# Kernel tuning notes

Hardware: AMD Instinct MI355X
Metric: run time of the kernel (lower is better)

## Reference

```python
import math
import jax
import jax.numpy as jnp
import numpy as np

SEGMENT_SIZE = 2048   # w (init: segment_size)
DILATION_RATE = 4     # r (init: dilation_rate)
D_MODEL = 1024        # init: d_model


def _sparse_indices(n: int, w: int, r: int, head_idx: int) -> np.ndarray:
    """Static SparsifyIndices: per segment of size w, take tokens offset::r.
    Since r divides w, every segment yields exactly m=w//r indices (no -1 pad).
    Returns flat global token indices, shape (S*m,)."""
    S = n // w
    m = w // r
    off = head_idx % r
    seg_start = np.arange(S, dtype=np.int64)[:, None] * w      # (S,1)
    within = off + r * np.arange(m, dtype=np.int64)[None, :]   # (1,m)
    return (seg_start + within).reshape(-1)


def setup_inputs() -> dict:
    key = jax.random.key(0)
    x = jax.random.normal(key, (4, 8192, D_MODEL), dtype=jnp.float32)
    return {"x": x, "head_idx": 1}


def reference(x, head_idx):
    b, n0, d = x.shape
    w, r = SEGMENT_SIZE, DILATION_RATE
    pad = (-n0) % w
    if pad:
        x = jnp.pad(x, ((0, 0), (0, pad), (0, 0)))
    n = n0 + pad
    idx = _sparse_indices(n, w, r, int(head_idx))  # static, (S*m,)
    S, m = n // w, w // r

    # Gather dilated tokens per segment: (b, S, m, d)
    xg = x[:, idx, :].reshape(b, S, m, d)

    # Softmax attention within each sub-segment (q=k=v=xg)
    scores = jnp.einsum('bsid,bsjd->bsij', xg, xg) / math.sqrt(d)  # (b,S,m,m)
    probs = jax.nn.softmax(scores, axis=-1)
    att = jnp.einsum('bsij,bsjd->bsid', probs, xg).reshape(b, S * m, d)

    # MixOutputs: alpha-weighted scatter-add back to full sequence
    denoms = att.sum(-1)                                       # (b, S*m)
    denom_sums = jnp.zeros((b, n), x.dtype).at[:, idx].add(denoms)
    alphas = denoms / denom_sums[:, idx]                       # (b, S*m)
    out = jnp.zeros((b, n, d), x.dtype).at[:, idx, :].add(att * alphas[..., None])
    return out
```

## Files before the change

### kernel.cpp

```cpp
#include <hip/hip_runtime.h>
#include <hip/hip_bf16.h>


typedef __bf16 bf16_t;
typedef __bf16 bf16x8 __attribute__((ext_vector_type(8)));
typedef float floatx4 __attribute__((ext_vector_type(4)));

#define D_MODEL 1024
#define SEG_W   2048
#define RATE    4
#define M_SUB   512
#define NTOK    8192
#define NSEGT   16
#define XG_ELEMS ((long)NSEGT * M_SUB * D_MODEL)

__device__ __forceinline__ void gload16(const bf16_t* g, bf16_t* l) {
    __builtin_amdgcn_global_load_lds(
        (const __attribute__((address_space(1))) void*)g,
        (__attribute__((address_space(3))) void*)l, 16, 0, 0);
}

__global__ __launch_bounds__(256) void gather_kernel(
    const float* __restrict__ x, const int* __restrict__ hidp,
    bf16_t* __restrict__ xg, bf16_t* __restrict__ xgT)
{
    const int off = ((hidp[0] % RATE) + RATE) % RATE;
    const int bid = blockIdx.x;
    const int seg = bid >> 7;
    const int rem = bid & 127;
    const int it  = rem >> 4;
    const int dt  = rem & 15;
    const int b   = seg >> 2, s = seg & 3;

    __shared__ ushort tile[64][65];

    const int t  = threadIdx.x;
    const int r  = t >> 2;
    const int cq = (t & 3) << 4;

    union U8 { bf16x8 v; ushort u[8]; };

    {
        const int  i   = it * 64 + r;
        const long tok = (long)s * SEG_W + off + 4L * i;
        const float* src = x + ((long)b * NTOK + tok) * D_MODEL + dt * 64 + cq;
        float4 f0 = ((const float4*)src)[0];
        float4 f1 = ((const float4*)src)[1];
        float4 f2 = ((const float4*)src)[2];
        float4 f3 = ((const float4*)src)[3];
        U8 lo, hi;
        lo.v[0]=(bf16_t)f0.x; lo.v[1]=(bf16_t)f0.y; lo.v[2]=(bf16_t)f0.z; lo.v[3]=(bf16_t)f0.w;
        lo.v[4]=(bf16_t)f1.x; lo.v[5]=(bf16_t)f1.y; lo.v[6]=(bf16_t)f1.z; lo.v[7]=(bf16_t)f1.w;
        hi.v[0]=(bf16_t)f2.x; hi.v[1]=(bf16_t)f2.y; hi.v[2]=(bf16_t)f2.z; hi.v[3]=(bf16_t)f2.w;
        hi.v[4]=(bf16_t)f3.x; hi.v[5]=(bf16_t)f3.y; hi.v[6]=(bf16_t)f3.z; hi.v[7]=(bf16_t)f3.w;
        bf16_t* dstg = xg + ((long)seg * M_SUB + i) * D_MODEL + dt * 64 + cq;
        *(bf16x8*)(dstg)     = lo.v;
        *(bf16x8*)(dstg + 8) = hi.v;
        #pragma unroll
        for (int j = 0; j < 8; ++j) { tile[r][cq + j] = lo.u[j]; tile[r][cq + 8 + j] = hi.u[j]; }
    }
    __syncthreads();
    {
        const int dc = r;
        const int iq = cq;
        U8 o0, o1;
        #pragma unroll
        for (int j = 0; j < 8; ++j) { o0.u[j] = tile[iq + j][dc]; o1.u[j] = tile[iq + 8 + j][dc]; }
        bf16_t* dstT = xgT + ((long)seg * D_MODEL + dt * 64 + dc) * M_SUB + it * 64 + iq;
        *(bf16x8*)(dstT)     = o0.v;
        *(bf16x8*)(dstT + 8) = o1.v;
    }
}

__global__ __launch_bounds__(256) void qk_kernel(
    const bf16_t* __restrict__ xg, bf16_t* __restrict__ S)
{
    const int bid = blockIdx.x;
    const int seg = bid >> 5;
    const int mt  = (bid >> 2) & 7;
    const int nt  = bid & 3;

    const int tid  = threadIdx.x;
    const int w    = tid >> 6;
    const int lane = tid & 63;
    const int l16  = lane & 15;
    const int quad = lane >> 4;
    const int wr   = w >> 1, wc = w & 1;
    const int rowin = lane >> 3;
    const int cswz  = ((lane & 7) ^ rowin) * 8;
    const int rsw   = l16 & 7;

    __shared__ alignas(16) bf16_t As[64 * 64];
    __shared__ alignas(16) bf16_t Bs[128 * 64];

    const bf16_t* xseg = xg + (long)seg * M_SUB * D_MODEL;

    const bf16_t* ga0 = xseg + (long)(mt * 64 + w * 16 + rowin) * D_MODEL + cswz;
    const bf16_t* ga1 = ga0 + 8 * D_MODEL;
    const bf16_t* gb0 = xseg + (long)(nt * 128 + w * 32 + rowin) * D_MODEL + cswz;
    const bf16_t* gb1 = gb0 +  8 * D_MODEL;
    const bf16_t* gb2 = gb0 + 16 * D_MODEL;
    const bf16_t* gb3 = gb0 + 24 * D_MODEL;
    bf16_t* la0 = &As[(w * 16 + 0) * 64];
    bf16_t* la1 = &As[(w * 16 + 8) * 64];
    bf16_t* lb0 = &Bs[(w * 32 + 0) * 64];
    bf16_t* lb1 = &Bs[(w * 32 + 8) * 64];
    bf16_t* lb2 = &Bs[(w * 32 + 16) * 64];
    bf16_t* lb3 = &Bs[(w * 32 + 24) * 64];

    floatx4 acc[2][4];
    #pragma unroll
    for (int i = 0; i < 2; ++i)
        #pragma unroll
        for (int j = 0; j < 4; ++j) acc[i][j] = (floatx4){0.f, 0.f, 0.f, 0.f};

    for (int kk = 0; kk < D_MODEL; kk += 64) {
        __syncthreads();
        gload16(ga0 + kk, la0); gload16(ga1 + kk, la1);
        gload16(gb0 + kk, lb0); gload16(gb1 + kk, lb1);
        gload16(gb2 + kk, lb2); gload16(gb3 + kk, lb3);
        __syncthreads();

        #pragma unroll
        for (int ks = 0; ks < 2; ++ks) {
            bf16x8 Af[2], Bf[4];
            #pragma unroll
            for (int m2 = 0; m2 < 2; ++m2) {
                const int row = wr * 32 + m2 * 16 + l16;
                Af[m2] = *(const bf16x8*)&As[row * 64 + (((ks * 4 + quad) ^ rsw) * 8)];
            }
            #pragma unroll
            for (int n2 = 0; n2 < 4; ++n2) {
                const int row = wc * 64 + n2 * 16 + l16;
                Bf[n2] = *(const bf16x8*)&Bs[row * 64 + (((ks * 4 + quad) ^ rsw) * 8)];
            }
            #pragma unroll
            for (int m2 = 0; m2 < 2; ++m2)
                #pragma unroll
                for (int n2 = 0; n2 < 4; ++n2)
                    acc[m2][n2] = __builtin_amdgcn_mfma_f32_16x16x32_bf16(Af[m2], Bf[n2], acc[m2][n2], 0, 0, 0);
        }
    }

    const float scale = 0.03125f;
    bf16_t* Sseg = S + (long)seg * M_SUB * M_SUB;
    #pragma unroll
    for (int m2 = 0; m2 < 2; ++m2) {
        const int qrow = mt * 64 + wr * 32 + m2 * 16 + quad * 4;
        #pragma unroll
        for (int n2 = 0; n2 < 4; ++n2) {
            const int col = nt * 128 + wc * 64 + n2 * 16 + l16;
            #pragma unroll
            for (int rg = 0; rg < 4; ++rg)
                Sseg[(long)(qrow + rg) * M_SUB + col] = (bf16_t)(acc[m2][n2][rg] * scale);
        }
    }
}

__global__ __launch_bounds__(256) void softmax_kernel(bf16_t* __restrict__ S)
{
    const int row  = blockIdx.x * 4 + (threadIdx.x >> 6);
    const int lane = threadIdx.x & 63;
    bf16_t* p = S + (long)row * M_SUB + lane * 8;
    bf16x8 v = *(const bf16x8*)p;
    float f[8];
    #pragma unroll
    for (int j = 0; j < 8; ++j) f[j] = (float)v[j];
    float m = f[0];
    #pragma unroll
    for (int j = 1; j < 8; ++j) m = fmaxf(m, f[j]);
    #pragma unroll
    for (int d = 1; d < 64; d <<= 1) m = fmaxf(m, __shfl_xor(m, d, 64));
    float sum = 0.f;
    #pragma unroll
    for (int j = 0; j < 8; ++j) { f[j] = __expf(f[j] - m); sum += f[j]; }
    #pragma unroll
    for (int d = 1; d < 64; d <<= 1) sum += __shfl_xor(sum, d, 64);
    const float inv = 1.0f / sum;
    #pragma unroll
    for (int j = 0; j < 8; ++j) v[j] = (bf16_t)(f[j] * inv);
    *(bf16x8*)p = v;
}

__global__ __launch_bounds__(256) void pv_kernel(
    const bf16_t* __restrict__ S, const bf16_t* __restrict__ xgT,
    const int* __restrict__ hidp, float* __restrict__ out)
{
    const int off = ((hidp[0] % RATE) + RATE) % RATE;
    const int bid = blockIdx.x;
    const int seg = bid >> 5;
    const int mt  = (bid >> 3) & 3;
    const int nt  = bid & 7;
    const int b   = seg >> 2, s = seg & 3;

    const int tid  = threadIdx.x;
    const int w    = tid >> 6;
    const int lane = tid & 63;
    const int l16  = lane & 15;
    const int quad = lane >> 4;
    const int wr   = w >> 1, wc = w & 1;
    const int rowin = lane >> 3;
    const int cswz  = ((lane & 7) ^ rowin) * 8;
    const int rsw   = l16 & 7;

    __shared__ alignas(16) bf16_t As[128 * 64];
    __shared__ alignas(16) bf16_t Bs[128 * 64];

    const bf16_t* Aseg = S   + (long)seg * M_SUB * M_SUB  + (long)mt * 128 * M_SUB;
    const bf16_t* Bseg = xgT + (long)seg * D_MODEL * M_SUB + (long)nt * 128 * M_SUB;

    const bf16_t* ga0 = Aseg + (long)(w * 32 + rowin) * M_SUB + cswz;
    const bf16_t* ga1 = ga0 +  8 * M_SUB;
    const bf16_t* ga2 = ga0 + 16 * M_SUB;
    const bf16_t* ga3 = ga0 + 24 * M_SUB;
    const bf16_t* gb0 = Bseg + (long)(w * 32 + rowin) * M_SUB + cswz;
    const bf16_t* gb1 = gb0 +  8 * M_SUB;
    const bf16_t* gb2 = gb0 + 16 * M_SUB;
    const bf16_t* gb3 = gb0 + 24 * M_SUB;
    bf16_t* la0 = &As[(w * 32 + 0) * 64];
    bf16_t* la1 = &As[(w * 32 + 8) * 64];
    bf16_t* la2 = &As[(w * 32 + 16) * 64];
    bf16_t* la3 = &As[(w * 32 + 24) * 64];
    bf16_t* lb0 = &Bs[(w * 32 + 0) * 64];
    bf16_t* lb1 = &Bs[(w * 32 + 8) * 64];
    bf16_t* lb2 = &Bs[(w * 32 + 16) * 64];
    bf16_t* lb3 = &Bs[(w * 32 + 24) * 64];

    floatx4 acc[4][4];
    #pragma unroll
    for (int i = 0; i < 4; ++i)
        #pragma unroll
        for (int j = 0; j < 4; ++j) acc[i][j] = (floatx4){0.f, 0.f, 0.f, 0.f};

    for (int kk = 0; kk < M_SUB; kk += 64) {
        __syncthreads();
        gload16(ga0 + kk, la0); gload16(ga1 + kk, la1);
        gload16(ga2 + kk, la2); gload16(ga3 + kk, la3);
        gload16(gb0 + kk, lb0); gload16(gb1 + kk, lb1);
        gload16(gb2 + kk, lb2); gload16(gb3 + kk, lb3);
        __syncthreads();

        #pragma unroll
        for (int ks = 0; ks < 2; ++ks) {
            bf16x8 Af[4], Bf[4];
            #pragma unroll
            for (int m2 = 0; m2 < 4; ++m2) {
                const int row = wr * 64 + m2 * 16 + l16;
                Af[m2] = *(const bf16x8*)&As[row * 64 + (((ks * 4 + quad) ^ rsw) * 8)];
            }
            #pragma unroll
            for (int n2 = 0; n2 < 4; ++n2) {
                const int row = wc * 64 + n2 * 16 + l16;
                Bf[n2] = *(const bf16x8*)&Bs[row * 64 + (((ks * 4 + quad) ^ rsw) * 8)];
            }
            #pragma unroll
            for (int m2 = 0; m2 < 4; ++m2)
                #pragma unroll
                for (int n2 = 0; n2 < 4; ++n2)
                    acc[m2][n2] = __builtin_amdgcn_mfma_f32_16x16x32_bf16(Af[m2], Bf[n2], acc[m2][n2], 0, 0, 0);
        }
    }

    float* obase = out + (long)b * NTOK * D_MODEL;
    #pragma unroll
    for (int m2 = 0; m2 < 4; ++m2) {
        const int qrow0 = mt * 128 + wr * 64 + m2 * 16 + quad * 4;
        #pragma unroll
        for (int rg = 0; rg < 4; ++rg) {
            const long tok = (long)s * SEG_W + off + 4L * (qrow0 + rg);
            float* orow = obase + tok * D_MODEL;
            #pragma unroll
            for (int n2 = 0; n2 < 4; ++n2) {
                const int d = nt * 128 + wc * 64 + n2 * 16 + l16;
                __builtin_nontemporal_store(acc[m2][n2][rg], &orow[d]);
            }
        }
    }

    {
        const floatx4 z = {0.f, 0.f, 0.f, 0.f};
        const int zr = tid >> 5;
        const int zc = tid & 31;
        #pragma unroll 4
        for (int p = 0; p < 48; ++p) {
            const int j = p * 8 + zr;
            const int q = j / 3, e = j % 3;
            const int delta = e + (e >= off ? 1 : 0);
            const long tok = (long)s * SEG_W + 4L * (mt * 128 + q) + delta;
            float* dst = obase + tok * D_MODEL + nt * 128 + zc * 4;
            __builtin_nontemporal_store(z, (floatx4*)dst);
        }
    }
}

extern "C" void kernel_launch(void* const* d_in, const int* in_sizes, int n_in,
                              void* d_out, int out_size, void* d_ws, size_t ws_size,
                              hipStream_t stream) {
    const float* x   = (const float*)d_in[0];
    const int*   hid = (const int*)d_in[1];
    float*       out = (float*)d_out;
    bf16_t* xg  = (bf16_t*)d_ws;
    bf16_t* xgT = xg + XG_ELEMS;
    bf16_t* S   = xgT + XG_ELEMS;

    gather_kernel<<<dim3(2048), dim3(256), 0, stream>>>(x, hid, xg, xgT);
    qk_kernel<<<dim3(512), dim3(256), 0, stream>>>(xg, S);
    softmax_kernel<<<dim3(2048), dim3(256), 0, stream>>>(S);
    pv_kernel<<<dim3(512), dim3(256), 0, stream>>>(S, xgT, hid, out);
}
```

Baseline: 251.1 us.

## Double-buffer LDS tiles in QK and PV GEMMs and remap block order

Both GEMM kernels switch to double-buffered shared-memory tiles: the next K-slice is loaded with global_load_lds while MFMAs consume the current buffer, with one barrier per iteration instead of two. The block index is also permuted so consecutive workgroups come from different segments, which changes how blocks spread across XCDs and their L2 caches. The aim is to hide global-load latency behind compute. In exchange, LDS use doubles, which may lower occupancy. Correctness relies on the async LDS loads having completed at the single barrier.

```diff
diff --git a/kernel.cpp b/kernel.cpp
--- a/kernel.cpp
+++ b/kernel.cpp
@@ -75,7 +75,8 @@
 __global__ __launch_bounds__(256) void qk_kernel(
     const bf16_t* __restrict__ xg, bf16_t* __restrict__ S)
 {
-    const int bid = blockIdx.x;
+    const int bid0 = blockIdx.x;
+    const int bid  = ((bid0 & 7) << 6) | (bid0 >> 3);
     const int seg = bid >> 5;
     const int mt  = (bid >> 2) & 7;
     const int nt  = bid & 3;
@@ -90,8 +91,8 @@
     const int cswz  = ((lane & 7) ^ rowin) * 8;
     const int rsw   = l16 & 7;
 
-    __shared__ alignas(16) bf16_t As[64 * 64];
-    __shared__ alignas(16) bf16_t Bs[128 * 64];
+    __shared__ alignas(16) bf16_t As[2][64 * 64];
+    __shared__ alignas(16) bf16_t Bs[2][128 * 64];
 
     const bf16_t* xseg = xg + (long)seg * M_SUB * D_MODEL;
 
@@ -101,12 +102,9 @@
     const bf16_t* gb1 = gb0 +  8 * D_MODEL;
     const bf16_t* gb2 = gb0 + 16 * D_MODEL;
     const bf16_t* gb3 = gb0 + 24 * D_MODEL;
-    bf16_t* la0 = &As[(w * 16 + 0) * 64];
-    bf16_t* la1 = &As[(w * 16 + 8) * 64];
-    bf16_t* lb0 = &Bs[(w * 32 + 0) * 64];
-    bf16_t* lb1 = &Bs[(w * 32 + 8) * 64];
-    bf16_t* lb2 = &Bs[(w * 32 + 16) * 64];
-    bf16_t* lb3 = &Bs[(w * 32 + 24) * 64];
+    const int la0 = (w * 16 + 0) * 64, la1 = (w * 16 + 8) * 64;
+    const int lb0 = (w * 32 + 0) * 64, lb1 = (w * 32 + 8) * 64;
+    const int lb2 = (w * 32 + 16) * 64, lb3 = (w * 32 + 24) * 64;
 
     floatx4 acc[2][4];
     #pragma unroll
@@ -114,25 +112,34 @@
         #pragma unroll
         for (int j = 0; j < 4; ++j) acc[i][j] = (floatx4){0.f, 0.f, 0.f, 0.f};
 
-    for (int kk = 0; kk < D_MODEL; kk += 64) {
-        __syncthreads();
-        gload16(ga0 + kk, la0); gload16(ga1 + kk, la1);
-        gload16(gb0 + kk, lb0); gload16(gb1 + kk, lb1);
-        gload16(gb2 + kk, lb2); gload16(gb3 + kk, lb3);
-        __syncthreads();
-
+    gload16(ga0, &As[0][la0]); gload16(ga1, &As[0][la1]);
+    gload16(gb0, &Bs[0][lb0]); gload16(gb1, &Bs[0][lb1]);
+    gload16(gb2, &Bs[0][lb2]); gload16(gb3, &Bs[0][lb3]);
+    __syncthreads();
+
+    for (int t = 0; t < 16; ++t) {
+        const int cur = t & 1;
+        if (t < 15) {
+            const int kk = (t + 1) * 64;
+            const int nx = cur ^ 1;
+            gload16(ga0 + kk, &As[nx][la0]); gload16(ga1 + kk, &As[nx][la1]);
+            gload16(gb0 + kk, &Bs[nx][lb0]); gload16(gb1 + kk, &Bs[nx][lb1]);
+            gload16(gb2 + kk, &Bs[nx][lb2]); gload16(gb3 + kk, &Bs[nx][lb3]);
+        }
+        const bf16_t* Ab = As[cur];
+        const bf16_t* Bb = Bs[cur];
         #pragma unroll
         for (int ks = 0; ks < 2; ++ks) {
             bf16x8 Af[2], Bf[4];
             #pragma unroll
             for (int m2 = 0; m2 < 2; ++m2) {
                 const int row = wr * 32 + m2 * 16 + l16;
-                Af[m2] = *(const bf16x8*)&As[row * 64 + (((ks * 4 + quad) ^ rsw) * 8)];
+                Af[m2] = *(const bf16x8*)&Ab[row * 64 + (((ks * 4 + quad) ^ rsw) * 8)];
             }
             #pragma unroll
             for (int n2 = 0; n2 < 4; ++n2) {
                 const int row = wc * 64 + n2 * 16 + l16;
-                Bf[n2] = *(const bf16x8*)&Bs[row * 64 + (((ks * 4 + quad) ^ rsw) * 8)];
+                Bf[n2] = *(const bf16x8*)&Bb[row * 64 + (((ks * 4 + quad) ^ rsw) * 8)];
             }
             #pragma unroll
             for (int m2 = 0; m2 < 2; ++m2)
@@ -140,6 +147,7 @@
                 for (int n2 = 0; n2 < 4; ++n2)
                     acc[m2][n2] = __builtin_amdgcn_mfma_f32_16x16x32_bf16(Af[m2], Bf[n2], acc[m2][n2], 0, 0, 0);
         }
+        __syncthreads();
     }
 
     const float scale = 0.03125f;
@@ -187,7 +195,8 @@
     const int* __restrict__ hidp, float* __restrict__ out)
 {
     const int off = ((hidp[0] % RATE) + RATE) % RATE;
-    const int bid = blockIdx.x;
+    const int bid0 = blockIdx.x;
+    const int bid  = ((bid0 & 7) << 6) | (bid0 >> 3);
     const int seg = bid >> 5;
     const int mt  = (bid >> 3) & 3;
     const int nt  = bid & 7;
@@ -203,8 +212,8 @@
     const int cswz  = ((lane & 7) ^ rowin) * 8;
     const int rsw   = l16 & 7;
 
-    __shared__ alignas(16) bf16_t As[128 * 64];
-    __shared__ alignas(16) bf16_t Bs[128 * 64];
+    __shared__ alignas(16) bf16_t As[2][128 * 64];
+    __shared__ alignas(16) bf16_t Bs[2][128 * 64];
 
     const bf16_t* Aseg = S   + (long)seg * M_SUB * M_SUB  + (long)mt * 128 * M_SUB;
     const bf16_t* Bseg = xgT + (long)seg * D_MODEL * M_SUB + (long)nt * 128 * M_SUB;
@@ -217,14 +226,8 @@
     const bf16_t* gb1 = gb0 +  8 * M_SUB;
     const bf16_t* gb2 = gb0 + 16 * M_SUB;
     const bf16_t* gb3 = gb0 + 24 * M_SUB;
-    bf16_t* la0 = &As[(w * 32 + 0) * 64];
-    bf16_t* la1 = &As[(w * 32 + 8) * 64];
-    bf16_t* la2 = &As[(w * 32 + 16) * 64];
-    bf16_t* la3 = &As[(w * 32 + 24) * 64];
-    bf16_t* lb0 = &Bs[(w * 32 + 0) * 64];
-    bf16_t* lb1 = &Bs[(w * 32 + 8) * 64];
-    bf16_t* lb2 = &Bs[(w * 32 + 16) * 64];
-    bf16_t* lb3 = &Bs[(w * 32 + 24) * 64];
+    const int la0 = (w * 32 + 0) * 64, la1 = (w * 32 + 8) * 64;
+    const int la2 = (w * 32 + 16) * 64, la3 = (w * 32 + 24) * 64;
 
     floatx4 acc[4][4];
     #pragma unroll
@@ -232,26 +235,36 @@
         #pragma unroll
         for (int j = 0; j < 4; ++j) acc[i][j] = (floatx4){0.f, 0.f, 0.f, 0.f};
 
-    for (int kk = 0; kk < M_SUB; kk += 64) {
-        __syncthreads();
-        gload16(ga0 + kk, la0); gload16(ga1 + kk, la1);
-        gload16(ga2 + kk, la2); gload16(ga3 + kk, la3);
-        gload16(gb0 + kk, lb0); gload16(gb1 + kk, lb1);
-        gload16(gb2 + kk, lb2); gload16(gb3 + kk, lb3);
-        __syncthreads();
-
+    gload16(ga0, &As[0][la0]); gload16(ga1, &As[0][la1]);
+    gload16(ga2, &As[0][la2]); gload16(ga3, &As[0][la3]);
+    gload16(gb0, &Bs[0][la0]); gload16(gb1, &Bs[0][la1]);
+    gload16(gb2, &Bs[0][la2]); gload16(gb3, &Bs[0][la3]);
+    __syncthreads();
+
+    for (int t = 0; t < 8; ++t) {
+        const int cur = t & 1;
+        if (t < 7) {
+            const int kk = (t + 1) * 64;
+            const int nx = cur ^ 1;
+            gload16(ga0 + kk, &As[nx][la0]); gload16(ga1 + kk, &As[nx][la1]);
+            gload16(ga2 + kk, &As[nx][la2]); gload16(ga3 + kk, &As[nx][la3]);
+            gload16(gb0 + kk, &Bs[nx][la0]); gload16(gb1 + kk, &Bs[nx][la1]);
+            gload16(gb2 + kk, &Bs[nx][la2]); gload16(gb3 + kk, &Bs[nx][la3]);
+        }
+        const bf16_t* Ab = As[cur];
+        const bf16_t* Bb = Bs[cur];
         #pragma unroll
         for (int ks = 0; ks < 2; ++ks) {
             bf16x8 Af[4], Bf[4];
             #pragma unroll
             for (int m2 = 0; m2 < 4; ++m2) {
                 const int row = wr * 64 + m2 * 16 + l16;
-                Af[m2] = *(const bf16x8*)&As[row * 64 + (((ks * 4 + quad) ^ rsw) * 8)];
+                Af[m2] = *(const bf16x8*)&Ab[row * 64 + (((ks * 4 + quad) ^ rsw) * 8)];
             }
             #pragma unroll
             for (int n2 = 0; n2 < 4; ++n2) {
                 const int row = wc * 64 + n2 * 16 + l16;
-                Bf[n2] = *(const bf16x8*)&Bs[row * 64 + (((ks * 4 + quad) ^ rsw) * 8)];
+                Bf[n2] = *(const bf16x8*)&Bb[row * 64 + (((ks * 4 + quad) ^ rsw) * 8)];
             }
             #pragma unroll
             for (int m2 = 0; m2 < 4; ++m2)
@@ -259,6 +272,7 @@
                 for (int n2 = 0; n2 < 4; ++n2)
                     acc[m2][n2] = __builtin_amdgcn_mfma_f32_16x16x32_bf16(Af[m2], Bf[n2], acc[m2][n2], 0, 0, 0);
         }
+        __syncthreads();
     }
 
     float* obase = out + (long)b * NTOK * D_MODEL;
```

Measured after the change: 253.6 us. Within noise of the previous version (+1.0%).

## Fuse QK, softmax and PV into a single attention kernel per query band

Applied to the files above, without the earlier changes.

Replaces the separate QK, softmax and PV kernels with one fused kernel. Each 512-thread block owns a 32-row query band, computes the full score row across 8 waves, and does the softmax with cross-wave max/sum reductions in shared memory. It keeps the probabilities in LDS for the PV matmul, so the bf16 score matrix no longer makes a round trip through global memory and two kernel launches are dropped. The fused kernel loads operands directly from global into registers with software double-buffering instead of staging them through LDS. The cost is K/V re-reads from global/L2 per band and a launch of only 256 blocks.

```diff
diff --git a/kernel.cpp b/kernel.cpp
--- a/kernel.cpp
+++ b/kernel.cpp
@@ -13,12 +13,6 @@
 #define NTOK    8192
 #define NSEGT   16
 #define XG_ELEMS ((long)NSEGT * M_SUB * D_MODEL)
-
-__device__ __forceinline__ void gload16(const bf16_t* g, bf16_t* l) {
-    __builtin_amdgcn_global_load_lds(
-        (const __attribute__((address_space(1))) void*)g,
-        (__attribute__((address_space(3))) void*)l, 16, 0, 0);
-}
 
 __global__ __launch_bounds__(256) void gather_kernel(
     const float* __restrict__ x, const int* __restrict__ hidp,
@@ -72,223 +66,223 @@
     }
 }
 
-__global__ __launch_bounds__(256) void qk_kernel(
-    const bf16_t* __restrict__ xg, bf16_t* __restrict__ S)
+__global__ __launch_bounds__(512) void attn_kernel(
+    const bf16_t* __restrict__ xg, const bf16_t* __restrict__ xgT,
+    const int* __restrict__ hidp, float* __restrict__ out)
 {
-    const int bid = blockIdx.x;
-    const int seg = bid >> 5;
-    const int mt  = (bid >> 2) & 7;
-    const int nt  = bid & 3;
+    const int off  = ((hidp[0] % RATE) + RATE) % RATE;
+    const int bid0 = blockIdx.x;
+    const int sub  = bid0 >> 3;
+    const int seg  = (bid0 & 7) * 2 + (sub >> 4);
+    const int band = sub & 15;
+    const int b = seg >> 2, s = seg & 3;
 
     const int tid  = threadIdx.x;
     const int w    = tid >> 6;
     const int lane = tid & 63;
     const int l16  = lane & 15;
     const int quad = lane >> 4;
-    const int wr   = w >> 1, wc = w & 1;
-    const int rowin = lane >> 3;
-    const int cswz  = ((lane & 7) ^ rowin) * 8;
-    const int rsw   = l16 & 7;
-
-    __shared__ alignas(16) bf16_t As[64 * 64];
-    __shared__ alignas(16) bf16_t Bs[128 * 64];
-
-    const bf16_t* xseg = xg + (long)seg * M_SUB * D_MODEL;
-
-    const bf16_t* ga0 = xseg + (long)(mt * 64 + w * 16 + rowin) * D_MODEL + cswz;
-    const bf16_t* ga1 = ga0 + 8 * D_MODEL;
-    const bf16_t* gb0 = xseg + (long)(nt * 128 + w * 32 + rowin) * D_MODEL + cswz;
-    const bf16_t* gb1 = gb0 +  8 * D_MODEL;
-    const bf16_t* gb2 = gb0 + 16 * D_MODEL;
-    const bf16_t* gb3 = gb0 + 24 * D_MODEL;
-    bf16_t* la0 = &As[(w * 16 + 0) * 64];
-    bf16_t* la1 = &As[(w * 16 + 8) * 64];
-    bf16_t* lb0 = &Bs[(w * 32 + 0) * 64];
-    bf16_t* lb1 = &Bs[(w * 32 + 8) * 64];
-    bf16_t* lb2 = &Bs[(w * 32 + 16) * 64];
-    bf16_t* lb3 = &Bs[(w * 32 + 24) * 64];
-
-    floatx4 acc[2][4];
-    #pragma unroll
-    for (int i = 0; i < 2; ++i)
-        #pragma unroll
-        for (int j = 0; j < 4; ++j) acc[i][j] = (floatx4){0.f, 0.f, 0.f, 0.f};
-
-    for (int kk = 0; kk < D_MODEL; kk += 64) {
-        __syncthreads();
-        gload16(ga0 + kk, la0); gload16(ga1 + kk, la1);
-        gload16(gb0 + kk, lb0); gload16(gb1 + kk, lb1);
-        gload16(gb2 + kk, lb2); gload16(gb3 + kk, lb3);
-        __syncthreads();
-
-        #pragma unroll
-        for (int ks = 0; ks < 2; ++ks) {
-            bf16x8 Af[2], Bf[4];
-            #pragma unroll
-            for (int m2 = 0; m2 < 2; ++m2) {
-                const int row = wr * 32 + m2 * 16 + l16;
-                Af[m2] = *(const bf16x8*)&As[row * 64 + (((ks * 4 + quad) ^ rsw) * 8)];
+
+    __shared__ alignas(16) bf16_t P_lds[32 * 512];
+    __shared__ float redmax[8][32];
+    __shared__ float redsum[8][32];
+
+    const bf16_t* xs  = xg + (long)seg * M_SUB * D_MODEL;
+    const bf16_t* qa0 = xs + (long)(band * 32 + l16) * D_MODEL + quad * 8;
+    const bf16_t* qa1 = qa0 + 16 * D_MODEL;
+    const bf16_t* kb0 = xs + (long)(w * 64 + l16) * D_MODEL + quad * 8;
+    const bf16_t* kb1 = kb0 + 16 * D_MODEL;
+    const bf16_t* kb2 = kb0 + 32 * D_MODEL;
+    const bf16_t* kb3 = kb0 + 48 * D_MODEL;
+
+    floatx4 acc_s[2][4];
+    #pragma unroll
+    for (int m = 0; m < 2; ++m)
+        #pragma unroll
+        for (int n = 0; n < 4; ++n) acc_s[m][n] = (floatx4){0.f, 0.f, 0.f, 0.f};
+
+    auto lqk = [&](int st, bf16x8 (&A)[2], bf16x8 (&B)[4]) {
+        const int o = st * 32;
+        A[0] = *(const bf16x8*)(qa0 + o); A[1] = *(const bf16x8*)(qa1 + o);
+        B[0] = *(const bf16x8*)(kb0 + o); B[1] = *(const bf16x8*)(kb1 + o);
+        B[2] = *(const bf16x8*)(kb2 + o); B[3] = *(const bf16x8*)(kb3 + o);
+    };
+    auto mqk = [&](bf16x8 (&A)[2], bf16x8 (&B)[4]) {
+        #pragma unroll
+        for (int m = 0; m < 2; ++m)
+            #pragma unroll
+            for (int n = 0; n < 4; ++n)
+                acc_s[m][n] = __builtin_amdgcn_mfma_f32_16x16x32_bf16(A[m], B[n], acc_s[m][n], 0, 0, 0);
+    };
+
+    {
+        bf16x8 aP[2], bP[4], aN[2], bN[4];
+        lqk(0, aP, bP);
+        #pragma unroll 4
+        for (int st = 0; st < 32; st += 2) {
+            lqk(st + 1, aN, bN);
+            mqk(aP, bP);
+            if (st + 2 < 32) lqk(st + 2, aP, bP);
+            mqk(aN, bN);
+        }
+    }
+
+    #pragma unroll
+    for (int m = 0; m < 2; ++m)
+        #pragma unroll
+        for (int n = 0; n < 4; ++n)
+            #pragma unroll
+            for (int rg = 0; rg < 4; ++rg) acc_s[m][n][rg] *= 0.03125f;
+
+    float mx[2][4];
+    #pragma unroll
+    for (int m = 0; m < 2; ++m)
+        #pragma unroll
+        for (int rg = 0; rg < 4; ++rg)
+            mx[m][rg] = fmaxf(fmaxf(acc_s[m][0][rg], acc_s[m][1][rg]),
+                              fmaxf(acc_s[m][2][rg], acc_s[m][3][rg]));
+    #pragma unroll
+    for (int d = 1; d < 16; d <<= 1)
+        #pragma unroll
+        for (int m = 0; m < 2; ++m)
+            #pragma unroll
+            for (int rg = 0; rg < 4; ++rg)
+                mx[m][rg] = fmaxf(mx[m][rg], __shfl_xor(mx[m][rg], d, 64));
+    if (l16 == 0) {
+        #pragma unroll
+        for (int m = 0; m < 2; ++m)
+            #pragma unroll
+            for (int rg = 0; rg < 4; ++rg)
+                redmax[w][m * 16 + quad * 4 + rg] = mx[m][rg];
+    }
+    __syncthreads();
+    float gm[2][4];
+    #pragma unroll
+    for (int m = 0; m < 2; ++m)
+        #pragma unroll
+        for (int rg = 0; rg < 4; ++rg) {
+            const int row = m * 16 + quad * 4 + rg;
+            float g = redmax[0][row];
+            #pragma unroll
+            for (int ww = 1; ww < 8; ++ww) g = fmaxf(g, redmax[ww][row]);
+            gm[m][rg] = g;
+        }
+    float sm[2][4] = {{0.f,0.f,0.f,0.f},{0.f,0.f,0.f,0.f}};
+    #pragma unroll
+    for (int m = 0; m < 2; ++m)
+        #pragma unroll
+        for (int n = 0; n < 4; ++n)
+            #pragma unroll
+            for (int rg = 0; rg < 4; ++rg) {
+                const float e = __expf(acc_s[m][n][rg] - gm[m][rg]);
+                acc_s[m][n][rg] = e;
+                sm[m][rg] += e;
             }
-            #pragma unroll
-            for (int n2 = 0; n2 < 4; ++n2) {
-                const int row = wc * 64 + n2 * 16 + l16;
-                Bf[n2] = *(const bf16x8*)&Bs[row * 64 + (((ks * 4 + quad) ^ rsw) * 8)];
+    #pragma unroll
+    for (int d = 1; d < 16; d <<= 1)
+        #pragma unroll
+        for (int m = 0; m < 2; ++m)
+            #pragma unroll
+            for (int rg = 0; rg < 4; ++rg)
+                sm[m][rg] += __shfl_xor(sm[m][rg], d, 64);
+    if (l16 == 0) {
+        #pragma unroll
+        for (int m = 0; m < 2; ++m)
+            #pragma unroll
+            for (int rg = 0; rg < 4; ++rg)
+                redsum[w][m * 16 + quad * 4 + rg] = sm[m][rg];
+    }
+    __syncthreads();
+    float iv[2][4];
+    #pragma unroll
+    for (int m = 0; m < 2; ++m)
+        #pragma unroll
+        for (int rg = 0; rg < 4; ++rg) {
+            const int row = m * 16 + quad * 4 + rg;
+            float t = redsum[0][row];
+            #pragma unroll
+            for (int ww = 1; ww < 8; ++ww) t += redsum[ww][row];
+            iv[m][rg] = 1.f / t;
+        }
+
+    #pragma unroll
+    for (int m = 0; m < 2; ++m)
+        #pragma unroll
+        for (int rg = 0; rg < 4; ++rg) {
+            const int row = m * 16 + quad * 4 + rg;
+            const float f = iv[m][rg];
+            #pragma unroll
+            for (int n = 0; n < 4; ++n) {
+                const int col = w * 64 + n * 16 + l16;
+                const int sw  = (((col >> 3) ^ (row & 7)) << 3) + (col & 7);
+                P_lds[row * 512 + sw] = (bf16_t)(acc_s[m][n][rg] * f);
             }
-            #pragma unroll
-            for (int m2 = 0; m2 < 2; ++m2)
-                #pragma unroll
-                for (int n2 = 0; n2 < 4; ++n2)
-                    acc[m2][n2] = __builtin_amdgcn_mfma_f32_16x16x32_bf16(Af[m2], Bf[n2], acc[m2][n2], 0, 0, 0);
-        }
-    }
-
-    const float scale = 0.03125f;
-    bf16_t* Sseg = S + (long)seg * M_SUB * M_SUB;
-    #pragma unroll
-    for (int m2 = 0; m2 < 2; ++m2) {
-        const int qrow = mt * 64 + wr * 32 + m2 * 16 + quad * 4;
-        #pragma unroll
-        for (int n2 = 0; n2 < 4; ++n2) {
-            const int col = nt * 128 + wc * 64 + n2 * 16 + l16;
-            #pragma unroll
-            for (int rg = 0; rg < 4; ++rg)
-                Sseg[(long)(qrow + rg) * M_SUB + col] = (bf16_t)(acc[m2][n2][rg] * scale);
-        }
-    }
-}
-
-__global__ __launch_bounds__(256) void softmax_kernel(bf16_t* __restrict__ S)
-{
-    const int row  = blockIdx.x * 4 + (threadIdx.x >> 6);
-    const int lane = threadIdx.x & 63;
-    bf16_t* p = S + (long)row * M_SUB + lane * 8;
-    bf16x8 v = *(const bf16x8*)p;
-    float f[8];
-    #pragma unroll
-    for (int j = 0; j < 8; ++j) f[j] = (float)v[j];
-    float m = f[0];
-    #pragma unroll
-    for (int j = 1; j < 8; ++j) m = fmaxf(m, f[j]);
-    #pragma unroll
-    for (int d = 1; d < 64; d <<= 1) m = fmaxf(m, __shfl_xor(m, d, 64));
-    float sum = 0.f;
-    #pragma unroll
-    for (int j = 0; j < 8; ++j) { f[j] = __expf(f[j] - m); sum += f[j]; }
-    #pragma unroll
-    for (int d = 1; d < 64; d <<= 1) sum += __shfl_xor(sum, d, 64);
-    const float inv = 1.0f / sum;
-    #pragma unroll
-    for (int j = 0; j < 8; ++j) v[j] = (bf16_t)(f[j] * inv);
-    *(bf16x8*)p = v;
-}
-
-__global__ __launch_bounds__(256) void pv_kernel(
-    const bf16_t* __restrict__ S, const bf16_t* __restrict__ xgT,
-    const int* __restrict__ hidp, float* __restrict__ out)
-{
-    const int off = ((hidp[0] % RATE) + RATE) % RATE;
-    const int bid = blockIdx.x;
-    const int seg = bid >> 5;
-    const int mt  = (bid >> 3) & 3;
-    const int nt  = bid & 7;
-    const int b   = seg >> 2, s = seg & 3;
-
-    const int tid  = threadIdx.x;
-    const int w    = tid >> 6;
-    const int lane = tid & 63;
-    const int l16  = lane & 15;
-    const int quad = lane >> 4;
-    const int wr   = w >> 1, wc = w & 1;
-    const int rowin = lane >> 3;
-    const int cswz  = ((lane & 7) ^ rowin) * 8;
-    const int rsw   = l16 & 7;
-
-    __shared__ alignas(16) bf16_t As[128 * 64];
-    __shared__ alignas(16) bf16_t Bs[128 * 64];
-
-    const bf16_t* Aseg = S   + (long)seg * M_SUB * M_SUB  + (long)mt * 128 * M_SUB;
-    const bf16_t* Bseg = xgT + (long)seg * D_MODEL * M_SUB + (long)nt * 128 * M_SUB;
-
-    const bf16_t* ga0 = Aseg + (long)(w * 32 + rowin) * M_SUB + cswz;
-    const bf16_t* ga1 = ga0 +  8 * M_SUB;
-    const bf16_t* ga2 = ga0 + 16 * M_SUB;
-    const bf16_t* ga3 = ga0 + 24 * M_SUB;
-    const bf16_t* gb0 = Bseg + (long)(w * 32 + rowin) * M_SUB + cswz;
-    const bf16_t* gb1 = gb0 +  8 * M_SUB;
-    const bf16_t* gb2 = gb0 + 16 * M_SUB;
-    const bf16_t* gb3 = gb0 + 24 * M_SUB;
-    bf16_t* la0 = &As[(w * 32 + 0) * 64];
-    bf16_t* la1 = &As[(w * 32 + 8) * 64];
-    bf16_t* la2 = &As[(w * 32 + 16) * 64];
-    bf16_t* la3 = &As[(w * 32 + 24) * 64];
-    bf16_t* lb0 = &Bs[(w * 32 + 0) * 64];
-    bf16_t* lb1 = &Bs[(w * 32 + 8) * 64];
-    bf16_t* lb2 = &Bs[(w * 32 + 16) * 64];
-    bf16_t* lb3 = &Bs[(w * 32 + 24) * 64];
-
-    floatx4 acc[4][4];
-    #pragma unroll
-    for (int i = 0; i < 4; ++i)
-        #pragma unroll
-        for (int j = 0; j < 4; ++j) acc[i][j] = (floatx4){0.f, 0.f, 0.f, 0.f};
-
-    for (int kk = 0; kk < M_SUB; kk += 64) {
-        __syncthreads();
-        gload16(ga0 + kk, la0); gload16(ga1 + kk, la1);
-        gload16(ga2 + kk, la2); gload16(ga3 + kk, la3);
-        gload16(gb0 + kk, lb0); gload16(gb1 + kk, lb1);
-        gload16(gb2 + kk, lb2); gload16(gb3 + kk, lb3);
-        __syncthreads();
-
-        #pragma unroll
-        for (int ks = 0; ks < 2; ++ks) {
-            bf16x8 Af[4], Bf[4];
-            #pragma unroll
-            for (int m2 = 0; m2 < 4; ++m2) {
-                const int row = wr * 64 + m2 * 16 + l16;
-                Af[m2] = *(const bf16x8*)&As[row * 64 + (((ks * 4 + quad) ^ rsw) * 8)];
-            }
-            #pragma unroll
-            for (int n2 = 0; n2 < 4; ++n2) {
-                const int row = wc * 64 + n2 * 16 + l16;
-                Bf[n2] = *(const bf16x8*)&Bs[row * 64 + (((ks * 4 + quad) ^ rsw) * 8)];
-            }
-            #pragma unroll
-            for (int m2 = 0; m2 < 4; ++m2)
-                #pragma unroll
-                for (int n2 = 0; n2 < 4; ++n2)
-                    acc[m2][n2] = __builtin_amdgcn_mfma_f32_16x16x32_bf16(Af[m2], Bf[n2], acc[m2][n2], 0, 0, 0);
+        }
+    __syncthreads();
+
+    floatx4 acc_o[2][8];
+    #pragma unroll
+    for (int m = 0; m < 2; ++m)
+        #pragma unroll
+        for (int n = 0; n < 8; ++n) acc_o[m][n] = (floatx4){0.f, 0.f, 0.f, 0.f};
+
+    const bf16_t* vb = xgT + ((long)seg * D_MODEL + w * 128 + l16) * M_SUB + quad * 8;
+
+    auto lpv = [&](int kt, bf16x8 (&A)[2], bf16x8 (&B)[8]) {
+        #pragma unroll
+        for (int m = 0; m < 2; ++m) {
+            const int row = m * 16 + l16;
+            const int ch  = (kt * 4 + quad) ^ (l16 & 7);
+            A[m] = *(const bf16x8*)&P_lds[row * 512 + ch * 8];
+        }
+        const int ko = kt * 32;
+        #pragma unroll
+        for (int n = 0; n < 8; ++n)
+            B[n] = *(const bf16x8*)(vb + (long)n * 16 * M_SUB + ko);
+    };
+    auto mpv = [&](bf16x8 (&A)[2], bf16x8 (&B)[8]) {
+        #pragma unroll
+        for (int m = 0; m < 2; ++m)
+            #pragma unroll
+            for (int n = 0; n < 8; ++n)
+                acc_o[m][n] = __builtin_amdgcn_mfma_f32_16x16x32_bf16(A[m], B[n], acc_o[m][n], 0, 0, 0);
+    };
+
+    {
+        bf16x8 aP[2], bP[8], aN[2], bN[8];
+        lpv(0, aP, bP);
+        #pragma unroll 2
+        for (int kt = 0; kt < 16; kt += 2) {
+            lpv(kt + 1, aN, bN);
+            mpv(aP, bP);
+            if (kt + 2 < 16) lpv(kt + 2, aP, bP);
+            mpv(aN, bN);
         }
     }
 
     float* obase = out + (long)b * NTOK * D_MODEL;
     #pragma unroll
-    for (int m2 = 0; m2 < 4; ++m2) {
-        const int qrow0 = mt * 128 + wr * 64 + m2 * 16 + quad * 4;
+    for (int m = 0; m < 2; ++m)
         #pragma unroll
         for (int rg = 0; rg < 4; ++rg) {
-            const long tok = (long)s * SEG_W + off + 4L * (qrow0 + rg);
-            float* orow = obase + tok * D_MODEL;
-            #pragma unroll
-            for (int n2 = 0; n2 < 4; ++n2) {
-                const int d = nt * 128 + wc * 64 + n2 * 16 + l16;
-                __builtin_nontemporal_store(acc[m2][n2][rg], &orow[d]);
-            }
-        }
-    }
+            const long tok = (long)s * SEG_W + off + 4L * (band * 32 + m * 16 + quad * 4 + rg);
+            float* orow = obase + tok * D_MODEL + w * 128 + l16;
+            #pragma unroll
+            for (int n = 0; n < 8; ++n)
+                __builtin_nontemporal_store(acc_o[m][n][rg], orow + n * 16);
+        }
 
     {
         const floatx4 z = {0.f, 0.f, 0.f, 0.f};
-        const int zr = tid >> 5;
-        const int zc = tid & 31;
+        const int chunk = tid & 255;
+        const int half  = tid >> 8;
         #pragma unroll 4
         for (int p = 0; p < 48; ++p) {
-            const int j = p * 8 + zr;
-            const int q = j / 3, e = j % 3;
+            const int t = p * 2 + half;
+            const int q = t / 3, e = t % 3;
             const int delta = e + (e >= off ? 1 : 0);
-            const long tok = (long)s * SEG_W + 4L * (mt * 128 + q) + delta;
-            float* dst = obase + tok * D_MODEL + nt * 128 + zc * 4;
-            __builtin_nontemporal_store(z, (floatx4*)dst);
+            const long tok = (long)s * SEG_W + 4L * (band * 32 + q) + delta;
+            __builtin_nontemporal_store(z, (floatx4*)(obase + tok * D_MODEL + chunk * 4));
         }
     }
 }
@@ -301,10 +295,7 @@
     float*       out = (float*)d_out;
     bf16_t* xg  = (bf16_t*)d_ws;
     bf16_t* xgT = xg + XG_ELEMS;
-    bf16_t* S   = xgT + XG_ELEMS;
 
     gather_kernel<<<dim3(2048), dim3(256), 0, stream>>>(x, hid, xg, xgT);
-    qk_kernel<<<dim3(512), dim3(256), 0, stream>>>(xg, S);
-    softmax_kernel<<<dim3(2048), dim3(256), 0, stream>>>(S);
-    pv_kernel<<<dim3(512), dim3(256), 0, stream>>>(S, xgT, hid, out);
+    attn_kernel<<<dim3(256), dim3(512), 0, stream>>>(xg, xgT, hid, out);
 }
```

New measurement: 288.5 us. 1.15x slower.
